# Kernel optimization log

Hardware: AMD Instinct MI355X
Metric: run time of the kernel (lower is better)

The kernel has to match this reference:

```python
import jax, jax.numpy as jnp
import numpy as np
import math
from jax import lax


def setup_inputs() -> dict:
    key = jax.random.key(0)
    k1, k2, k3 = jax.random.split(key, 3)
    B, C, H, W = 32, 64, 224, 224
    padding, stride, k_size = 0, 2, 2
    p_height, p_width = 32, 32
    Ho = (H + 2 * padding - k_size) // stride + 1
    Wo = (W + 2 * padding - k_size) // stride + 1
    in_tensor = jax.random.normal(k1, (B, C, H, W), dtype=jnp.float32)
    # persistent previously-computed pooled output (stale state)
    out_tensor = jax.random.normal(k2, (B, C, Ho, Wo), dtype=jnp.float32)
    patch_location_tensor = jax.random.randint(k3, (B, 2), 0, H - p_height, dtype=jnp.int32)
    return {
        "in_tensor": in_tensor,
        "out_tensor": out_tensor,
        "patch_location_tensor": patch_location_tensor,
        "padding": padding,
        "stride": stride,
        "k_size": k_size,
        "p_height": p_height,
        "p_width": p_width,
    }


def reference(in_tensor, out_tensor, patch_location_tensor,
              padding, stride, k_size, p_height, p_width):
    """Incremental max pool: recompute only the output window affected by a
    (p_height x p_width) dirty patch located per-image at patch_location_tensor
    (top-left, input coordinates), scatter it into the persistent out_tensor,
    and return updated output patch locations (output coordinates)."""
    B, C, H, W = in_tensor.shape
    _, _, Ho, Wo = out_tensor.shape
    # static output-patch extent (matches module's math.ceil formula)
    out_ph = int(math.ceil((p_height + k_size - 1) * 1.0 / stride))
    out_pw = int(math.ceil((p_width + k_size - 1) * 1.0 / stride))
    # input extent needed to compute that output window
    ext_h = (out_ph - 1) * stride + k_size
    ext_w = (out_pw - 1) * stride + k_size
    NEG = jnp.finfo(in_tensor.dtype).min
    # pad input with -inf so window maxima ignore padding
    x_pad = jnp.pad(in_tensor, ((0, 0), (0, 0), (padding, padding), (padding, padding)),
                    constant_values=NEG)

    def ceil_div(a, b):
        return -((-a) // b)

    def one_image(xp, prev_out, loc):
        # first output index touched by input row/col loc (padded coord loc+padding)
        oy = jnp.clip(ceil_div(loc[0] + padding - k_size + 1, stride), 0, Ho - out_ph)
        ox = jnp.clip(ceil_div(loc[1] + padding - k_size + 1, stride), 0, Wo - out_pw)
        patch = lax.dynamic_slice(xp, (0, oy * stride, ox * stride), (C, ext_h, ext_w))
        pooled = lax.reduce_window(patch, NEG, lax.max,
                                   (1, k_size, k_size), (1, stride, stride), 'VALID')
        new_out = lax.dynamic_update_slice(prev_out, pooled, (0, oy, ox))
        return new_out, jnp.stack([oy, ox]).astype(jnp.int32)

    new_out, new_loc = jax.vmap(one_image)(x_pad, out_tensor, patch_location_tensor)
    return new_out, new_loc
```

## Files before the change

kernel.cpp:

```cpp
#include <hip/hip_runtime.h>

#define BB 32
#define CC 64
#define HH 224
#define WW 224
#define HO 112
#define WO 112
#define OPH 17
#define OPW 17

__global__ void IncMaxPool_patch_kernel(const float* __restrict__ in,
                                        const int* __restrict__ loc,
                                        float* __restrict__ out) {
    const int bc = blockIdx.x;
    const int b = bc / CC;
    const int c = bc % CC;

    const int l0 = loc[b * 2 + 0];
    const int l1 = loc[b * 2 + 1];
    const int oy = min(max(l0 >> 1, 0), HO - OPH);
    const int ox = min(max(l1 >> 1, 0), WO - OPW);

    const float* __restrict__ ibase = in + (size_t)(b * CC + c) * HH * WW;
    float* __restrict__ obase = out + (size_t)(b * CC + c) * HO * WO;

    for (int idx = threadIdx.x; idx < OPH * OPW; idx += blockDim.x) {
        const int i = idx / OPW;
        const int j = idx - i * OPW;
        const int y = oy + i;
        const int x = ox + j;
        const float2 r0 = *(const float2*)(ibase + (size_t)(y * 2) * WW + x * 2);
        const float2 r1 = *(const float2*)(ibase + (size_t)(y * 2 + 1) * WW + x * 2);
        obase[y * WO + x] = fmaxf(fmaxf(r0.x, r0.y), fmaxf(r1.x, r1.y));
    }

    if (c == 0 && threadIdx.x == 0) {
        float* locout = out + (size_t)BB * CC * HO * WO;
        locout[b * 2 + 0] = (float)oy;
        locout[b * 2 + 1] = (float)ox;
    }
}

extern "C" void kernel_launch(void* const* d_in, const int* in_sizes, int n_in,
                              void* d_out, int out_size, void* d_ws, size_t ws_size,
                              hipStream_t stream) {
    const float* in_tensor  = (const float*)d_in[0];
    const float* out_tensor = (const float*)d_in[1];
    const int*   loc        = (const int*)d_in[2];
    float* out = (float*)d_out;

    const size_t bulk_bytes = (size_t)BB * CC * HO * WO * sizeof(float);
    hipMemcpyAsync(out, out_tensor, bulk_bytes, hipMemcpyDeviceToDevice, stream);

    IncMaxPool_patch_kernel<<<BB * CC, 256, 0, stream>>>(in_tensor, loc, out);
}
```

Before: 40.93 us.

## Fuse bulk output copy and patch max-pool into one float4 streaming kernel

Replaces the device-to-device memcpy plus separate patch kernel with a single kernel in which each thread copies one float4 of the previous output. Threads whose float4 overlaps the dirty patch recompute those elements from the input instead of keeping the stale values. This removes the second launch and the copy/kernel serialization and avoids writing the patch region twice. The cost is extra index arithmetic and some divergence in the threads that touch the patch.

```diff
diff --git a/kernel.cpp b/kernel.cpp
--- a/kernel.cpp
+++ b/kernel.cpp
@@ -9,35 +9,55 @@
 #define OPH 17
 #define OPW 17
 
-__global__ void IncMaxPool_patch_kernel(const float* __restrict__ in,
-                                        const int* __restrict__ loc,
-                                        float* __restrict__ out) {
-    const int bc = blockIdx.x;
-    const int b = bc / CC;
-    const int c = bc % CC;
+#define IMG_F4   (CC * HO * WO / 4)
+#define CH_F4    (HO * WO / 4)
+#define ROW_F4   (WO / 4)
+#define TOTAL_F4 (BB * IMG_F4)
+
+__global__ __launch_bounds__(256)
+void IncMaxPool_fused_kernel(const float* __restrict__ in,
+                             const float* __restrict__ prev,
+                             const int* __restrict__ loc,
+                             float* __restrict__ out) {
+    const int tid = blockIdx.x * 256 + threadIdx.x;
+
+    const int b  = tid / IMG_F4;
+    const int r0 = tid - b * IMG_F4;
+    const int c  = r0 / CH_F4;
+    const int r1 = r0 - c * CH_F4;
+    const int y  = r1 / ROW_F4;
+    const int x4 = (r1 - y * ROW_F4) * 4;
 
     const int l0 = loc[b * 2 + 0];
     const int l1 = loc[b * 2 + 1];
     const int oy = min(max(l0 >> 1, 0), HO - OPH);
     const int ox = min(max(l1 >> 1, 0), WO - OPW);
 
-    const float* __restrict__ ibase = in + (size_t)(b * CC + c) * HH * WW;
-    float* __restrict__ obase = out + (size_t)(b * CC + c) * HO * WO;
+    float4 v = ((const float4*)prev)[tid];
 
-    for (int idx = threadIdx.x; idx < OPH * OPW; idx += blockDim.x) {
-        const int i = idx / OPW;
-        const int j = idx - i * OPW;
-        const int y = oy + i;
-        const int x = ox + j;
-        const float2 r0 = *(const float2*)(ibase + (size_t)(y * 2) * WW + x * 2);
-        const float2 r1 = *(const float2*)(ibase + (size_t)(y * 2 + 1) * WW + x * 2);
-        obase[y * WO + x] = fmaxf(fmaxf(r0.x, r0.y), fmaxf(r1.x, r1.y));
+    if (y >= oy && y < oy + OPH && (x4 + 3) >= ox && x4 <= (ox + OPW - 1)) {
+        const float* ib = in + (size_t)(b * CC + c) * (HH * WW) + (size_t)(y * 2) * WW;
+        float r[4] = {v.x, v.y, v.z, v.w};
+        #pragma unroll
+        for (int j = 0; j < 4; ++j) {
+            const int x = x4 + j;
+            if (x >= ox && x < ox + OPW) {
+                const float2 a = *(const float2*)(ib + x * 2);
+                const float2 d = *(const float2*)(ib + WW + x * 2);
+                r[j] = fmaxf(fmaxf(a.x, a.y), fmaxf(d.x, d.y));
+            }
+        }
+        v = make_float4(r[0], r[1], r[2], r[3]);
     }
 
-    if (c == 0 && threadIdx.x == 0) {
+    ((float4*)out)[tid] = v;
+
+    if (tid < BB) {
+        const int m0 = loc[tid * 2 + 0];
+        const int m1 = loc[tid * 2 + 1];
         float* locout = out + (size_t)BB * CC * HO * WO;
-        locout[b * 2 + 0] = (float)oy;
-        locout[b * 2 + 1] = (float)ox;
+        locout[tid * 2 + 0] = (float)min(max(m0 >> 1, 0), HO - OPH);
+        locout[tid * 2 + 1] = (float)min(max(m1 >> 1, 0), WO - OPW);
     }
 }
 
@@ -49,8 +69,5 @@
     const int*   loc        = (const int*)d_in[2];
     float* out = (float*)d_out;
 
-    const size_t bulk_bytes = (size_t)BB * CC * HO * WO * sizeof(float);
-    hipMemcpyAsync(out, out_tensor, bulk_bytes, hipMemcpyDeviceToDevice, stream);
-
-    IncMaxPool_patch_kernel<<<BB * CC, 256, 0, stream>>>(in_tensor, loc, out);
+    IncMaxPool_fused_kernel<<<TOTAL_F4 / 256, 256, 0, stream>>>(in_tensor, out_tensor, loc, out);
 }
```

Result: faster. 38.25 us (-6.5%).
